# Kernel tuning notes

Hardware: AMD Instinct MI355X
Metric: run time of the kernel (lower is better)

## Reference

```python
import jax, jax.numpy as jnp
import numpy as np

B, N, D = 2, 2048, 1024
H, DH = 16, 64
DI = 4096
EPS = 1e-5
NEG_SLOPE = 0.01  # F.leaky_relu default


def _ln(x, g, b):
    mu = jnp.mean(x, axis=-1, keepdims=True)
    var = jnp.mean((x - mu) ** 2, axis=-1, keepdims=True)
    return (x - mu) * jax.lax.rsqrt(var + EPS) * g + b


def setup_inputs() -> dict:
    key = jax.random.key(0)
    ks = jax.random.split(key, 10)
    s = 0.02
    return {
        "Z": jax.random.normal(ks[0], (B, N, D), jnp.float32),
        "new_mask": jax.random.normal(ks[1], (B, N, N), jnp.float32),
        "mask": jax.random.uniform(ks[2], (B, N, N), jnp.float32),
        "ln1_g": jnp.ones((D,), jnp.float32),
        "ln1_b": jnp.zeros((D,), jnp.float32),
        "qkv_w": jax.random.normal(ks[3], (3 * D, D), jnp.float32) * s,
        "qkv_b": jnp.zeros((3 * D,), jnp.float32),
        "o_w": jax.random.normal(ks[4], (D, H * DH), jnp.float32) * s,
        "ln2_g": jnp.ones((D,), jnp.float32),
        "ln2_b": jnp.zeros((D,), jnp.float32),
        "p1_w": jax.random.normal(ks[5], (DI, D), jnp.float32) * s,
        "p1_b": jnp.zeros((DI,), jnp.float32),
        "p2_w": jax.random.normal(ks[6], (D, DI), jnp.float32) * s,
        "p2_b": jnp.zeros((D,), jnp.float32),
    }


def reference(Z, new_mask, mask, ln1_g, ln1_b, qkv_w, qkv_b, o_w, ln2_g, ln2_b, p1_w, p1_b, p2_w, p2_b):
    inp = Z
    Zn = _ln(Z, ln1_g, ln1_b)
    qkv = (Zn @ qkv_w.T + qkv_b).reshape(B, N, H, 3 * DH)
    # torch chunk order in the source: V, Q, K
    V, Q, K = jnp.split(qkv, 3, axis=3)  # each [B,N,H,DH]
    # scores: einsum('bnij,bmij->binm') == [B,H,N,N]
    W = jnp.einsum("bnhd,bmhd->bhnm", Q, K) / np.sqrt(DH) + new_mask[:, None]
    A = jax.nn.softmax(W, axis=3) * mask[:, None]
    attn = jnp.einsum("bhnm,bmhd->bnhd", A, V).reshape(B, N, D)
    attn = jnp.where(attn >= 0, attn, NEG_SLOPE * attn) @ o_w.T  # leaky_relu then o_net (no bias)
    Z1 = attn + inp
    Zn2 = _ln(Z1, ln2_g, ln2_b)
    h = jax.nn.relu(Zn2 @ p1_w.T + p1_b)
    return h @ p2_w.T + p2_b + Z1
```

## Files before the change

### kernel.cpp

```cpp
#include <hip/hip_runtime.h>

typedef unsigned short u16;
typedef __attribute__((ext_vector_type(8))) short bf16x8;
typedef __attribute__((ext_vector_type(4))) float f32x4;
typedef __attribute__((ext_vector_type(16))) float f32x16;
typedef __attribute__((ext_vector_type(4))) unsigned u32x4;

#define DEV static __device__ __forceinline__

DEV u16 f2bf(float f) {
    unsigned u = __float_as_uint(f);
    u += 0x7FFFu + ((u >> 16) & 1u);
    return (u16)(u >> 16);
}

typedef const __attribute__((address_space(1))) void* gas1_t;
typedef __attribute__((address_space(3))) void* gas3_t;

DEV void gl_lds16(const u16* g, u16* l) {
    __builtin_amdgcn_global_load_lds((gas1_t)g, (gas3_t)l, 16, 0, 0);
}

DEV unsigned cvtpk_bf16(float a, float b) {
    unsigned r;
    asm("v_cvt_pk_bf16_f32 %0, %1, %2" : "=v"(r) : "v"(a), "v"(b));
    return r;
}

DEV int sw8(int row, int chunk) { return row * 64 + ((chunk ^ (row & 7)) << 3); }

__global__ __launch_bounds__(256) void prep_all(const float* __restrict__ qkv_w,
                                                const float* __restrict__ o_w,
                                                const float* __restrict__ p1_w,
                                                const float* __restrict__ p2_w,
                                                const float* __restrict__ qkv_b,
                                                const float* __restrict__ nm,
                                                const float* __restrict__ pm,
                                                u16* __restrict__ qkvW,
                                                u16* __restrict__ oW,
                                                u16* __restrict__ p1W,
                                                u16* __restrict__ p2W,
                                                float* __restrict__ pbias,
                                                unsigned* __restrict__ Mp) {
    const int bid = blockIdx.x, t = threadIdx.x;
    if (bid < 3072) {
        int i = bid * 256 + t;
        int orow = i >> 8, cc = i & 255;
        int region = orow >> 10, rem = orow & 1023, h = rem >> 6, tt = rem & 63;
        int srow = h * 192 + region * 64 + tt;
        float4 v = ((const float4*)qkv_w)[srow * 256 + cc];
        ushort4 o;
        o.x = f2bf(v.x); o.y = f2bf(v.y); o.z = f2bf(v.z); o.w = f2bf(v.w);
        ((ushort4*)qkvW)[i] = o;
    } else if (bid < 4096) {
        int i = (bid - 3072) * 256 + t;
        float4 v = ((const float4*)o_w)[i];
        ushort4 o;
        o.x = f2bf(v.x); o.y = f2bf(v.y); o.z = f2bf(v.z); o.w = f2bf(v.w);
        ((ushort4*)oW)[i] = o;
    } else if (bid < 8192) {
        int i = (bid - 4096) * 256 + t;
        float4 v = ((const float4*)p1_w)[i];
        ushort4 o;
        o.x = f2bf(v.x); o.y = f2bf(v.y); o.z = f2bf(v.z); o.w = f2bf(v.w);
        ((ushort4*)p1W)[i] = o;
    } else if (bid < 12288) {
        int i = (bid - 8192) * 256 + t;
        float4 v = ((const float4*)p2_w)[i];
        ushort4 o;
        o.x = f2bf(v.x); o.y = f2bf(v.y); o.z = f2bf(v.z); o.w = f2bf(v.w);
        ((ushort4*)p2W)[i] = o;
    } else if (bid < 20480) {
        int i = (bid - 12288) * 256 + t;
        float4 a = ((const float4*)nm)[i];
        float4 b = ((const float4*)pm)[i];
        uint4 o;
        o.x = ((unsigned)f2bf(b.x) << 16) | f2bf(a.x * 1.4426950f);
        o.y = ((unsigned)f2bf(b.y) << 16) | f2bf(a.y * 1.4426950f);
        o.z = ((unsigned)f2bf(b.z) << 16) | f2bf(a.z * 1.4426950f);
        o.w = ((unsigned)f2bf(b.w) << 16) | f2bf(a.w * 1.4426950f);
        int e = i * 4;
        int bb = e >> 22;
        int rem = e & 4194303;
        int n = rem >> 11;
        int m = rem & 2047;
        int mt = m >> 5;
        int m5 = m & 31;
        int c = m5 >> 3;
        int hi = (m5 >> 2) & 1;
        size_t oi = (((size_t)(bb * 64 + mt) * 4 + c) * 2048 + n) * 2 + hi;
        ((uint4*)Mp)[oi] = o;
    } else {
#pragma unroll
        for (int k = 0; k < 12; k++) {
            int i = k * 256 + t;
            int region = i >> 10, rem = i & 1023, h = rem >> 6, tt = rem & 63;
            pbias[i] = qkv_b[h * 192 + region * 64 + tt];
        }
    }
}

__global__ __launch_bounds__(256) void ln_bf16(const float* __restrict__ x,
                                               const float* __restrict__ gam,
                                               const float* __restrict__ bet,
                                               u16* __restrict__ y) {
    const int row = blockIdx.x;
    const int t = threadIdx.x;
    const float4 v = ((const float4*)(x + (size_t)row * 1024))[t];
    float s = v.x + v.y + v.z + v.w;
    float ss = v.x * v.x + v.y * v.y + v.z * v.z + v.w * v.w;
#pragma unroll
    for (int o = 1; o < 64; o <<= 1) {
        s += __shfl_xor(s, o);
        ss += __shfl_xor(ss, o);
    }
    __shared__ float rs[4], rss[4];
    const int wave = t >> 6, lane = t & 63;
    if (lane == 0) { rs[wave] = s; rss[wave] = ss; }
    __syncthreads();
    const float tot = rs[0] + rs[1] + rs[2] + rs[3];
    const float totss = rss[0] + rss[1] + rss[2] + rss[3];
    const float mu = tot * (1.0f / 1024.0f);
    const float var = totss * (1.0f / 1024.0f) - mu * mu;
    const float rstd = rsqrtf(var + 1e-5f);
    const float4 g4 = ((const float4*)gam)[t];
    const float4 b4 = ((const float4*)bet)[t];
    ushort4 o;
    o.x = f2bf((v.x - mu) * rstd * g4.x + b4.x);
    o.y = f2bf((v.y - mu) * rstd * g4.y + b4.y);
    o.z = f2bf((v.z - mu) * rstd * g4.z + b4.z);
    o.w = f2bf((v.w - mu) * rstd * g4.w + b4.w);
    ((ushort4*)(y + (size_t)row * 1024))[t] = o;
}

__global__ __launch_bounds__(256) void ln2_comb4(const float* __restrict__ p0,
                                                 const float* __restrict__ p1,
                                                 const float* __restrict__ p2,
                                                 const float* __restrict__ p3,
                                                 const float* __restrict__ Z,
                                                 const float* __restrict__ gam,
                                                 const float* __restrict__ bet,
                                                 float* __restrict__ Z1,
                                                 u16* __restrict__ y) {
    const int row = blockIdx.x;
    const int t = threadIdx.x;
    const size_t off = (size_t)row * 256 + t;
    const float4 a = ((const float4*)p0)[off];
    const float4 c = ((const float4*)p1)[off];
    const float4 d = ((const float4*)p2)[off];
    const float4 e = ((const float4*)p3)[off];
    const float4 z = ((const float4*)Z)[off];
    float4 v;
    v.x = a.x + c.x + d.x + e.x + z.x;
    v.y = a.y + c.y + d.y + e.y + z.y;
    v.z = a.z + c.z + d.z + e.z + z.z;
    v.w = a.w + c.w + d.w + e.w + z.w;
    ((float4*)Z1)[off] = v;
    float s = v.x + v.y + v.z + v.w;
    float ss = v.x * v.x + v.y * v.y + v.z * v.z + v.w * v.w;
#pragma unroll
    for (int o = 1; o < 64; o <<= 1) {
        s += __shfl_xor(s, o);
        ss += __shfl_xor(ss, o);
    }
    __shared__ float rs[4], rss[4];
    const int wave = t >> 6, lane = t & 63;
    if (lane == 0) { rs[wave] = s; rss[wave] = ss; }
    __syncthreads();
    const float tot = rs[0] + rs[1] + rs[2] + rs[3];
    const float totss = rss[0] + rss[1] + rss[2] + rss[3];
    const float mu = tot * (1.0f / 1024.0f);
    const float var = totss * (1.0f / 1024.0f) - mu * mu;
    const float rstd = rsqrtf(var + 1e-5f);
    const float4 g4 = ((const float4*)gam)[t];
    const float4 b4 = ((const float4*)bet)[t];
    ushort4 o;
    o.x = f2bf((v.x - mu) * rstd * g4.x + b4.x);
    o.y = f2bf((v.y - mu) * rstd * g4.y + b4.y);
    o.z = f2bf((v.z - mu) * rstd * g4.z + b4.z);
    o.w = f2bf((v.w - mu) * rstd * g4.w + b4.w);
    ((ushort4*)(y + (size_t)row * 1024))[t] = o;
}

__global__ __launch_bounds__(256) void out_comb(const float* __restrict__ p0,
                                                const float* __restrict__ p1,
                                                const float* __restrict__ bias,
                                                const float* __restrict__ Z1,
                                                float* __restrict__ out) {
    int i = blockIdx.x * 256 + threadIdx.x;
    float4 a = ((const float4*)p0)[i];
    float4 c = ((const float4*)p1)[i];
    float4 z = ((const float4*)Z1)[i];
    float4 b = ((const float4*)bias)[i & 255];
    float4 o;
    o.x = a.x + c.x + z.x + b.x; o.y = a.y + c.y + z.y + b.y;
    o.z = a.z + c.z + z.z + b.z; o.w = a.w + c.w + z.w + b.w;
    ((float4*)out)[i] = o;
}

template <int EPI>
__global__ __launch_bounds__(256, 3) void gemm_bt(const u16* __restrict__ A,
                                                  const u16* __restrict__ Bt,
                                                  const float* __restrict__ bias,
                                                  void* __restrict__ out0,
                                                  void* __restrict__ out1,
                                                  void* __restrict__ out2,
                                                  int M, int N, int K, int ldk) {
    __shared__ __align__(16) u16 As[128 * 32];
    __shared__ __align__(16) u16 Bs[128 * 32];
    const int tid = threadIdx.x;
    const int wave = tid >> 6, lane = tid & 63;
    const int lhi = lane >> 4, llo = lane & 15;
    const int bx = blockIdx.x, by = blockIdx.y;
    const int kz = blockIdx.z * K;

    const int arow = wave * 32 + (lane >> 2);
    const int acol = (lane & 3) * 8;
    const u16* gA = A + (size_t)(by * 128 + arow) * ldk + kz + acol;
    const u16* gB = Bt + (size_t)(bx * 128 + arow) * ldk + kz + acol;
    u16* lA = As + wave * 1024 + lane * 8;
    u16* lB = Bs + wave * 1024 + lane * 8;

    const int wr = wave >> 1, wc = wave & 1;
    const f32x4 zero = {0.f, 0.f, 0.f, 0.f};
    f32x4 acc[4][4];
#pragma unroll
    for (int i = 0; i < 4; i++)
#pragma unroll
        for (int j = 0; j < 4; j++) acc[i][j] = zero;

    for (int k0 = 0; k0 < K; k0 += 32) {
        __syncthreads();
        gl_lds16(gA, lA);
        gl_lds16(gA + 16 * (size_t)ldk, lA + 512);
        gl_lds16(gB, lB);
        gl_lds16(gB + 16 * (size_t)ldk, lB + 512);
        gA += 32; gB += 32;
        __syncthreads();
        bf16x8 af[4], bfr[4];
#pragma unroll
        for (int i = 0; i < 4; i++)
            af[i] = *(const bf16x8*)(As + (wr * 64 + i * 16 + llo) * 32 + lhi * 8);
#pragma unroll
        for (int j = 0; j < 4; j++)
            bfr[j] = *(const bf16x8*)(Bs + (wc * 64 + j * 16 + llo) * 32 + lhi * 8);
#pragma unroll
        for (int i = 0; i < 4; i++)
#pragma unroll
            for (int j = 0; j < 4; j++)
                acc[i][j] = __builtin_amdgcn_mfma_f32_16x16x32_bf16(af[i], bfr[j], acc[i][j], 0, 0, 0);
    }

    const int rbase = by * 128 + wr * 64 + lhi * 4;
    const int cbase = bx * 128 + wc * 64 + llo;
    float* pout = nullptr;
    if constexpr (EPI == 4) {
        pout = (blockIdx.z < 2) ? ((float*)out0 + (size_t)blockIdx.z * M * N)
                                : ((float*)out1 + (size_t)(blockIdx.z - 2) * M * N);
    }
#pragma unroll
    for (int i = 0; i < 4; i++) {
#pragma unroll
        for (int j = 0; j < 4; j++) {
#pragma unroll
            for (int r = 0; r < 4; r++) {
                const int row = rbase + i * 16 + r;
                const int col = cbase + j * 16;
                float v = acc[i][j][r];
                if constexpr (EPI == 0) {
                    v += bias[col];
                    const int region = col >> 10;
                    const int c = col & 1023;
                    const int b = row >> 11, n = row & 2047;
                    if (region == 0) {
                        ((float*)out0)[(size_t)row * 1024 + c] = v;
                    } else {
                        const int h = c >> 6, t = c & 63;
                        u16* dst = (region == 1) ? (u16*)out1 : (u16*)out2;
                        dst[(((size_t)(b * 16 + h)) * 2048 + n) * 64 + t] = f2bf(v);
                    }
                } else if constexpr (EPI == 2) {
                    v += bias[col];
                    v = v > 0.f ? v : 0.f;
                    ((u16*)out0)[(size_t)row * N + col] = f2bf(v);
                } else {
                    pout[(size_t)row * N + col] = v;
                }
            }
        }
    }
}

__global__ __launch_bounds__(256) void vtrans(const float* __restrict__ Vsc,
                                              u16* __restrict__ Vt) {
    __shared__ u16 Ts[64 * 72];
    const int nt = blockIdx.x;
    const int bh = blockIdx.y;
    const int b = bh >> 4, h = bh & 15;
    const int t = threadIdx.x;
    const int n0 = nt * 64;
    const int nr = t >> 2;
    const int dq = (t & 3) * 16;
    const float* src = Vsc + ((size_t)(b * 2048 + n0 + nr)) * 1024 + h * 64 + dq;
    float4 v0 = ((const float4*)src)[0];
    float4 v1 = ((const float4*)src)[1];
    float4 v2 = ((const float4*)src)[2];
    float4 v3 = ((const float4*)src)[3];
    u16* c0 = Ts + nr;
    c0[(dq + 0) * 72]  = f2bf(v0.x); c0[(dq + 1) * 72]  = f2bf(v0.y);
    c0[(dq + 2) * 72]  = f2bf(v0.z); c0[(dq + 3) * 72]  = f2bf(v0.w);
    c0[(dq + 4) * 72]  = f2bf(v1.x); c0[(dq + 5) * 72]  = f2bf(v1.y);
    c0[(dq + 6) * 72]  = f2bf(v1.z); c0[(dq + 7) * 72]  = f2bf(v1.w);
    c0[(dq + 8) * 72]  = f2bf(v2.x); c0[(dq + 9) * 72]  = f2bf(v2.y);
    c0[(dq + 10) * 72] = f2bf(v2.z); c0[(dq + 11) * 72] = f2bf(v2.w);
    c0[(dq + 12) * 72] = f2bf(v3.x); c0[(dq + 13) * 72] = f2bf(v3.y);
    c0[(dq + 14) * 72] = f2bf(v3.z); c0[(dq + 15) * 72] = f2bf(v3.w);
    __syncthreads();
    const int d = t >> 2, n8 = (t & 3) * 16;
    u16* dstrow = Vt + ((size_t)bh * 64 + d) * 2048 + n0;
#pragma unroll
    for (int w = 0; w < 4; w++) {
        const int gi = (n8 >> 2) + w;
        const int g5 = gi & 7, blk = gi >> 3;
        const int pg = (g5 & 4) | ((g5 & 1) << 1) | ((g5 >> 1) & 1);
        *(uint2*)(dstrow + blk * 32 + pg * 4) = *(const uint2*)(Ts + d * 72 + n8 + w * 4);
    }
}

DEV void stage_kv(const u16* __restrict__ Kg, const u16* __restrict__ Vtg,
                  u16* ks, u16* vs, int bh, int m0, int wave, int lane) {
    const int l3 = lane >> 3, l7 = lane & 7;
    const int swcol = (l7 ^ l3) << 3;
#pragma unroll
    for (int s = 0; s < 2; s++) {
        const int row = wave * 16 + s * 8 + l3;
        gl_lds16(Kg + ((size_t)bh * 2048 + m0 + row) * 64 + swcol,
                 ks + wave * 1024 + s * 512 + lane * 8);
        gl_lds16(Vtg + ((size_t)bh * 64 + row) * 2048 + m0 + swcol,
                 vs + wave * 1024 + s * 512 + lane * 8);
    }
}

__global__ __launch_bounds__(256, 4) void attn_fused6(const u16* __restrict__ Qg,
                                                      const u16* __restrict__ Kg,
                                                      const u16* __restrict__ Vtg,
                                                      const unsigned* __restrict__ Mp,
                                                      u16* __restrict__ attnL) {
    __shared__ __align__(16) u16 Ks[2][64 * 64];
    __shared__ __align__(16) u16 Vs[2][64 * 64];
    __shared__ float lsh[2][32], lsh2[2][32];
    const int tid = threadIdx.x, wave = tid >> 6, lane = tid & 63;
    const int qh = wave & 1, wm = wave >> 1;
    const int hi = lane >> 5, l31 = lane & 31;
    const int pid = blockIdx.x;
    const int seq = pid >> 3;
    const int hh = seq & 15;
    const int g = (pid & 7) + (seq >> 4) * 8;
    const int b = g >> 5, qt = g & 31;
    const int bh = b * 16 + hh;
    const int q0 = qt * 64;

    stage_kv(Kg, Vtg, Ks[0], Vs[0], bh, 0, wave, lane);
    const int qrow = q0 + qh * 32 + l31;
    const u16* qptr = Qg + ((size_t)bh * 2048 + qrow) * 64 + hi * 8;
    bf16x8 qf[4];
#pragma unroll
    for (int ks = 0; ks < 4; ks++) qf[ks] = *(const bf16x8*)(qptr + ks * 16);

    const uint4* mb4 = (const uint4*)Mp + ((size_t)(b * 64 + wm) * 4) * 4096
                                        + (size_t)qrow * 2 + hi;

    const f32x16 z16 = {0.f,0.f,0.f,0.f,0.f,0.f,0.f,0.f,0.f,0.f,0.f,0.f,0.f,0.f,0.f,0.f};
    f32x16 accO[2];
    accO[0] = z16; accO[1] = z16;
    float lsum = 0.f;
    const float CS = 0.125f * 1.4426950f;
    __syncthreads();

    for (int t = 0; t < 32; t++) {
        const int cur = t & 1;
        const uint4* mp4 = mb4 + (size_t)t * 32768;
        const uint4 mva = mp4[0], mvb = mp4[4096], mvc = mp4[8192], mvd = mp4[12288];
        if (t < 31) stage_kv(Kg, Vtg, Ks[cur ^ 1], Vs[cur ^ 1], bh, (t + 1) * 64, wave, lane);

        const u16* ksb = Ks[cur];
        f32x16 sacc = z16;
        __builtin_amdgcn_s_setprio(1);
#pragma unroll
        for (int ks = 0; ks < 4; ks++) {
            const bf16x8 kf = *(const bf16x8*)(ksb + sw8(wm * 32 + l31, ks * 2 + hi));
            sacc = __builtin_amdgcn_mfma_f32_32x32x16_bf16(kf, qf[ks], sacc, 0, 0, 0);
        }
        __builtin_amdgcn_s_setprio(0);

        const unsigned mm[16] = {mva.x, mva.y, mva.z, mva.w, mvb.x, mvb.y, mvb.z, mvb.w,
                                 mvc.x, mvc.y, mvc.z, mvc.w, mvd.x, mvd.y, mvd.z, mvd.w};
        float p[16];
#pragma unroll
        for (int r = 0; r < 16; r++) {
            const unsigned u = mm[r];
            const float e = exp2f(fmaf(sacc[r], CS, __uint_as_float(u << 16)));
            lsum += e;
            p[r] = e * __uint_as_float(u & 0xFFFF0000u);
        }
        const u32x4 fa0 = {cvtpk_bf16(p[0], p[1]),  cvtpk_bf16(p[2], p[3]),
                           cvtpk_bf16(p[4], p[5]),  cvtpk_bf16(p[6], p[7])};
        const u32x4 fa1 = {cvtpk_bf16(p[8], p[9]),  cvtpk_bf16(p[10], p[11]),
                           cvtpk_bf16(p[12], p[13]), cvtpk_bf16(p[14], p[15])};
        const bf16x8 pa0 = __builtin_bit_cast(bf16x8, fa0);
        const bf16x8 pa1 = __builtin_bit_cast(bf16x8, fa1);

        const u16* vsb = Vs[cur];
        __builtin_amdgcn_s_setprio(1);
#pragma unroll
        for (int dh = 0; dh < 2; dh++) {
            const bf16x8 vf0 = *(const bf16x8*)(vsb + sw8(dh * 32 + l31, wm * 4 + hi));
            accO[dh] = __builtin_amdgcn_mfma_f32_32x32x16_bf16(pa0, vf0, accO[dh], 0, 0, 0);
            const bf16x8 vf1 = *(const bf16x8*)(vsb + sw8(dh * 32 + l31, wm * 4 + 2 + hi));
            accO[dh] = __builtin_amdgcn_mfma_f32_32x32x16_bf16(pa1, vf1, accO[dh], 0, 0, 0);
        }
        __builtin_amdgcn_s_setprio(0);
        __syncthreads();
    }

    const float lsum2 = lsum + __shfl_xor(lsum, 32);
    float* cb = (float*)&Ks[0][0];
    if (wm == 1) {
        float* dst = cb + (size_t)(qh * 64 + lane) * 32;
#pragma unroll
        for (int dh = 0; dh < 2; dh++)
#pragma unroll
            for (int c = 0; c < 4; c++) {
                const f32x4 v = {accO[dh][c * 4 + 0], accO[dh][c * 4 + 1],
                                 accO[dh][c * 4 + 2], accO[dh][c * 4 + 3]};
                *(f32x4*)(dst + dh * 16 + c * 4) = v;
            }
        if (lane < 32) lsh[qh][lane] = lsum2;
    }
    __syncthreads();
    if (wm == 0) {
        const float* src = cb + (size_t)(qh * 64 + lane) * 32;
        const float lt = lsum2 + lsh[qh][l31];
#pragma unroll
        for (int dh = 0; dh < 2; dh++)
#pragma unroll
            for (int c = 0; c < 16; c++)
                accO[dh][c] += src[dh * 16 + c];
        if (lane < 32) lsh2[qh][lane] = 1.0f / lt;
    }
    __syncthreads();
    if (wm == 0) {
#pragma unroll
        for (int r = 0; r < 16; r++) {
            const int ql = (r & 3) + 8 * (r >> 2) + 4 * hi;
            const float linv = lsh2[qh][ql];
            const int qg = q0 + qh * 32 + ql;
#pragma unroll
            for (int dh = 0; dh < 2; dh++) {
                float v = accO[dh][r] * linv;
                v = v >= 0.f ? v : 0.01f * v;
                attnL[((size_t)b * 2048 + qg) * 1024 + hh * 64 + dh * 32 + l31] = f2bf(v);
            }
        }
    }
}

extern "C" void kernel_launch(void* const* d_in, const int* in_sizes, int n_in,
                              void* d_out, int out_size, void* d_ws, size_t ws_size,
                              hipStream_t stream) {
    const float* Z     = (const float*)d_in[0];
    const float* nmask = (const float*)d_in[1];
    const float* pmask = (const float*)d_in[2];
    const float* ln1_g = (const float*)d_in[3];
    const float* ln1_b = (const float*)d_in[4];
    const float* qkv_w = (const float*)d_in[5];
    const float* qkv_b = (const float*)d_in[6];
    const float* o_w   = (const float*)d_in[7];
    const float* ln2_g = (const float*)d_in[8];
    const float* ln2_b = (const float*)d_in[9];
    const float* p1_w  = (const float*)d_in[10];
    const float* p1_b  = (const float*)d_in[11];
    const float* p2_w  = (const float*)d_in[12];
    const float* p2_b  = (const float*)d_in[13];
    float* out = (float*)d_out;

    char* w = (char*)d_ws;
    auto take = [&](size_t bytes) -> char* {
        char* p = w;
        w += (bytes + 255) & ~(size_t)255;
        return p;
    };
    u16* qkvW   = (u16*)take((size_t)3072 * 1024 * 2);
    u16* oW     = (u16*)take((size_t)1024 * 1024 * 2);
    u16* p1W    = (u16*)take((size_t)4096 * 1024 * 2);
    u16* p2W    = (u16*)take((size_t)1024 * 4096 * 2);
    u16* Zn     = (u16*)take((size_t)4096 * 1024 * 2);
    u16* Qb     = (u16*)take((size_t)32 * 2048 * 64 * 2);
    u16* Kb     = (u16*)take((size_t)32 * 2048 * 64 * 2);
    u16* Vt     = (u16*)take((size_t)32 * 64 * 2048 * 2);
    u16* attnL  = (u16*)take((size_t)4096 * 1024 * 2);
    float* Z1   = (float*)take((size_t)4096 * 1024 * 4);
    u16* hbuf   = (u16*)take((size_t)4096 * 4096 * 2);
    unsigned* Mp = (unsigned*)take((size_t)2 * 2048 * 2048 * 4);
    float* pbias = (float*)take((size_t)3072 * 4);
    float* Vsc    = (float*)hbuf;
    float* part01 = (float*)Mp;
    float* part23 = (float*)hbuf;

    prep_all<<<dim3(20481), 256, 0, stream>>>(qkv_w, o_w, p1_w, p2_w, qkv_b, nmask, pmask,
                                              qkvW, oW, p1W, p2W, pbias, Mp);
    ln_bf16<<<dim3(4096), 256, 0, stream>>>(Z, ln1_g, ln1_b, Zn);
    gemm_bt<0><<<dim3(24, 32), 256, 0, stream>>>(Zn, qkvW, pbias, Vsc, Qb, Kb, 4096, 3072, 1024, 1024);
    vtrans<<<dim3(32, 32), 256, 0, stream>>>(Vsc, Vt);
    attn_fused6<<<dim3(1024), 256, 0, stream>>>(Qb, Kb, Vt, Mp, attnL);
    gemm_bt<4><<<dim3(8, 32, 4), 256, 0, stream>>>(attnL, oW, nullptr, part01, part23, nullptr,
                                                   4096, 1024, 256, 1024);
    ln2_comb4<<<dim3(4096), 256, 0, stream>>>(part01, part01 + (size_t)4096 * 1024,
                                              part23, part23 + (size_t)4096 * 1024,
                                              Z, ln2_g, ln2_b, Z1, Zn);
    gemm_bt<2><<<dim3(32, 32), 256, 0, stream>>>(Zn, p1W, p1_b, hbuf, nullptr, nullptr,
                                                 4096, 4096, 1024, 1024);
    gemm_bt<4><<<dim3(8, 32, 2), 256, 0, stream>>>(hbuf, p2W, nullptr, part01, nullptr, nullptr,
                                                   4096, 1024, 2048, 4096);
    out_comb<<<dim3(4096), 256, 0, stream>>>(part01, part01 + (size_t)4096 * 1024, p2_b, Z1, out);
}
```

Measured before the change: 447.8 us.

## Fuse V transpose into QKV GEMM epilogue and restructure attention loop

The QKV GEMM epilogue now writes V directly as transposed, permuted bf16 into Vt, which removes the fp32 Vsc intermediate and the separate vtrans kernel. The attention kernel is unrolled by two with explicit double-buffered staging and mask prefetch one tile ahead. The additive mask is preloaded as the MFMA accumulator initial value, so the per-element fma is folded away. The mask is now prescaled by 8 instead of log2e, and the cross-wave combine uses an XOR-swizzled LDS layout to avoid bank conflicts. The risks are extra register pressure from the prefetched mask and possible precision changes from the new mask scaling.

```diff
diff --git a/kernel.cpp b/kernel.cpp
--- a/kernel.cpp
+++ b/kernel.cpp
@@ -2,6 +2,7 @@
 
 typedef unsigned short u16;
 typedef __attribute__((ext_vector_type(8))) short bf16x8;
+typedef __attribute__((ext_vector_type(2))) float f32x2;
 typedef __attribute__((ext_vector_type(4))) float f32x4;
 typedef __attribute__((ext_vector_type(16))) float f32x16;
 typedef __attribute__((ext_vector_type(4))) unsigned u32x4;
@@ -13,6 +14,8 @@
     u += 0x7FFFu + ((u >> 16) & 1u);
     return (u16)(u >> 16);
 }
+
+DEV float uaf(unsigned u) { return __uint_as_float(u); }
 
 typedef const __attribute__((address_space(1))) void* gas1_t;
 typedef __attribute__((address_space(3))) void* gas3_t;
@@ -75,10 +78,10 @@
         float4 a = ((const float4*)nm)[i];
         float4 b = ((const float4*)pm)[i];
         uint4 o;
-        o.x = ((unsigned)f2bf(b.x) << 16) | f2bf(a.x * 1.4426950f);
-        o.y = ((unsigned)f2bf(b.y) << 16) | f2bf(a.y * 1.4426950f);
-        o.z = ((unsigned)f2bf(b.z) << 16) | f2bf(a.z * 1.4426950f);
-        o.w = ((unsigned)f2bf(b.w) << 16) | f2bf(a.w * 1.4426950f);
+        o.x = ((unsigned)f2bf(b.x) << 16) | f2bf(a.x * 8.0f);
+        o.y = ((unsigned)f2bf(b.y) << 16) | f2bf(a.y * 8.0f);
+        o.z = ((unsigned)f2bf(b.z) << 16) | f2bf(a.z * 8.0f);
+        o.w = ((unsigned)f2bf(b.w) << 16) | f2bf(a.w * 8.0f);
         int e = i * 4;
         int bb = e >> 22;
         int rem = e & 4194303;
@@ -253,95 +256,77 @@
 
     const int rbase = by * 128 + wr * 64 + lhi * 4;
     const int cbase = bx * 128 + wc * 64 + llo;
-    float* pout = nullptr;
-    if constexpr (EPI == 4) {
-        pout = (blockIdx.z < 2) ? ((float*)out0 + (size_t)blockIdx.z * M * N)
-                                : ((float*)out1 + (size_t)(blockIdx.z - 2) * M * N);
-    }
-#pragma unroll
-    for (int i = 0; i < 4; i++) {
-#pragma unroll
-        for (int j = 0; j < 4; j++) {
-#pragma unroll
-            for (int r = 0; r < 4; r++) {
-                const int row = rbase + i * 16 + r;
-                const int col = cbase + j * 16;
-                float v = acc[i][j][r];
-                if constexpr (EPI == 0) {
-                    v += bias[col];
-                    const int region = col >> 10;
-                    const int c = col & 1023;
-                    const int b = row >> 11, n = row & 2047;
-                    if (region == 0) {
-                        ((float*)out0)[(size_t)row * 1024 + c] = v;
-                    } else {
+    if constexpr (EPI == 0) {
+        if (cbase < 1024) {
+#pragma unroll
+            for (int i = 0; i < 4; i++) {
+                const int row0 = rbase + i * 16;
+                const int bb = row0 >> 11, nn = row0 & 2047;
+                const int g5 = (nn >> 2) & 7;
+                const int pg = (g5 & 4) | ((g5 & 1) << 1) | ((g5 >> 1) & 1);
+                const int nnp = (nn & ~31) | (pg << 2);
+#pragma unroll
+                for (int j = 0; j < 4; j++) {
+                    const int col = cbase + j * 16;
+                    const float bv = bias[col];
+                    const int h = col >> 6, d = col & 63;
+                    ushort4 o4;
+                    o4.x = f2bf(acc[i][j][0] + bv);
+                    o4.y = f2bf(acc[i][j][1] + bv);
+                    o4.z = f2bf(acc[i][j][2] + bv);
+                    o4.w = f2bf(acc[i][j][3] + bv);
+                    *(ushort4*)((u16*)out0 + ((size_t)(bb * 16 + h) * 64 + d) * 2048 + nnp) = o4;
+                }
+            }
+        } else {
+#pragma unroll
+            for (int i = 0; i < 4; i++) {
+#pragma unroll
+                for (int j = 0; j < 4; j++) {
+#pragma unroll
+                    for (int r = 0; r < 4; r++) {
+                        const int row = rbase + i * 16 + r;
+                        const int col = cbase + j * 16;
+                        float v = acc[i][j][r] + bias[col];
+                        const int region = col >> 10;
+                        const int c = col & 1023;
+                        const int b = row >> 11, n = row & 2047;
                         const int h = c >> 6, t = c & 63;
                         u16* dst = (region == 1) ? (u16*)out1 : (u16*)out2;
                         dst[(((size_t)(b * 16 + h)) * 2048 + n) * 64 + t] = f2bf(v);
                     }
-                } else if constexpr (EPI == 2) {
-                    v += bias[col];
-                    v = v > 0.f ? v : 0.f;
-                    ((u16*)out0)[(size_t)row * N + col] = f2bf(v);
-                } else {
-                    pout[(size_t)row * N + col] = v;
                 }
             }
         }
-    }
-}
-
-__global__ __launch_bounds__(256) void vtrans(const float* __restrict__ Vsc,
-                                              u16* __restrict__ Vt) {
-    __shared__ u16 Ts[64 * 72];
-    const int nt = blockIdx.x;
-    const int bh = blockIdx.y;
-    const int b = bh >> 4, h = bh & 15;
-    const int t = threadIdx.x;
-    const int n0 = nt * 64;
-    const int nr = t >> 2;
-    const int dq = (t & 3) * 16;
-    const float* src = Vsc + ((size_t)(b * 2048 + n0 + nr)) * 1024 + h * 64 + dq;
-    float4 v0 = ((const float4*)src)[0];
-    float4 v1 = ((const float4*)src)[1];
-    float4 v2 = ((const float4*)src)[2];
-    float4 v3 = ((const float4*)src)[3];
-    u16* c0 = Ts + nr;
-    c0[(dq + 0) * 72]  = f2bf(v0.x); c0[(dq + 1) * 72]  = f2bf(v0.y);
-    c0[(dq + 2) * 72]  = f2bf(v0.z); c0[(dq + 3) * 72]  = f2bf(v0.w);
-    c0[(dq + 4) * 72]  = f2bf(v1.x); c0[(dq + 5) * 72]  = f2bf(v1.y);
-    c0[(dq + 6) * 72]  = f2bf(v1.z); c0[(dq + 7) * 72]  = f2bf(v1.w);
-    c0[(dq + 8) * 72]  = f2bf(v2.x); c0[(dq + 9) * 72]  = f2bf(v2.y);
-    c0[(dq + 10) * 72] = f2bf(v2.z); c0[(dq + 11) * 72] = f2bf(v2.w);
-    c0[(dq + 12) * 72] = f2bf(v3.x); c0[(dq + 13) * 72] = f2bf(v3.y);
-    c0[(dq + 14) * 72] = f2bf(v3.z); c0[(dq + 15) * 72] = f2bf(v3.w);
-    __syncthreads();
-    const int d = t >> 2, n8 = (t & 3) * 16;
-    u16* dstrow = Vt + ((size_t)bh * 64 + d) * 2048 + n0;
-#pragma unroll
-    for (int w = 0; w < 4; w++) {
-        const int gi = (n8 >> 2) + w;
-        const int g5 = gi & 7, blk = gi >> 3;
-        const int pg = (g5 & 4) | ((g5 & 1) << 1) | ((g5 >> 1) & 1);
-        *(uint2*)(dstrow + blk * 32 + pg * 4) = *(const uint2*)(Ts + d * 72 + n8 + w * 4);
-    }
-}
-
-DEV void stage_kv(const u16* __restrict__ Kg, const u16* __restrict__ Vtg,
-                  u16* ks, u16* vs, int bh, int m0, int wave, int lane) {
-    const int l3 = lane >> 3, l7 = lane & 7;
-    const int swcol = (l7 ^ l3) << 3;
-#pragma unroll
-    for (int s = 0; s < 2; s++) {
-        const int row = wave * 16 + s * 8 + l3;
-        gl_lds16(Kg + ((size_t)bh * 2048 + m0 + row) * 64 + swcol,
-                 ks + wave * 1024 + s * 512 + lane * 8);
-        gl_lds16(Vtg + ((size_t)bh * 64 + row) * 2048 + m0 + swcol,
-                 vs + wave * 1024 + s * 512 + lane * 8);
-    }
-}
-
-__global__ __launch_bounds__(256, 4) void attn_fused6(const u16* __restrict__ Qg,
+    } else {
+        float* pout = nullptr;
+        if constexpr (EPI == 4) {
+            pout = (blockIdx.z < 2) ? ((float*)out0 + (size_t)blockIdx.z * M * N)
+                                    : ((float*)out1 + (size_t)(blockIdx.z - 2) * M * N);
+        }
+#pragma unroll
+        for (int i = 0; i < 4; i++) {
+#pragma unroll
+            for (int j = 0; j < 4; j++) {
+#pragma unroll
+                for (int r = 0; r < 4; r++) {
+                    const int row = rbase + i * 16 + r;
+                    const int col = cbase + j * 16;
+                    float v = acc[i][j][r];
+                    if constexpr (EPI == 2) {
+                        v += bias[col];
+                        v = v > 0.f ? v : 0.f;
+                        ((u16*)out0)[(size_t)row * N + col] = f2bf(v);
+                    } else {
+                        pout[(size_t)row * N + col] = v;
+                    }
+                }
+            }
+        }
+    }
+}
+
+__global__ __launch_bounds__(256, 4) void attn_fused7(const u16* __restrict__ Qg,
                                                       const u16* __restrict__ Kg,
                                                       const u16* __restrict__ Vtg,
                                                       const unsigned* __restrict__ Mp,
@@ -360,7 +345,22 @@
     const int bh = b * 16 + hh;
     const int q0 = qt * 64;
 
-    stage_kv(Kg, Vtg, Ks[0], Vs[0], bh, 0, wave, lane);
+    const int l3 = lane >> 3, l7 = lane & 7;
+    const int swcol = (l7 ^ l3) << 3;
+    const int srow = wave * 16 + l3;
+    const u16* kp = Kg + ((size_t)bh * 2048 + srow) * 64 + swcol;
+    const u16* vp = Vtg + ((size_t)bh * 64 + srow) * 2048 + swcol;
+    u16* lKa = Ks[0] + wave * 1024 + lane * 8;
+    u16* lKb = Ks[1] + wave * 1024 + lane * 8;
+    u16* lVa = Vs[0] + wave * 1024 + lane * 8;
+    u16* lVb = Vs[1] + wave * 1024 + lane * 8;
+
+#define STAGE(LK, LV) do { \
+        gl_lds16(kp, LK); gl_lds16(kp + 512, (LK) + 512); \
+        gl_lds16(vp, LV); gl_lds16(vp + 16384, (LV) + 512); \
+        kp += 4096; vp += 64; } while (0)
+
+    STAGE(lKa, lVa);
     const int qrow = q0 + qh * 32 + l31;
     const u16* qptr = Qg + ((size_t)bh * 2048 + qrow) * 64 + hi * 8;
     bf16x8 qf[4];
@@ -369,83 +369,108 @@
 
     const uint4* mb4 = (const uint4*)Mp + ((size_t)(b * 64 + wm) * 4) * 4096
                                         + (size_t)qrow * 2 + hi;
+    uint4 mA0 = mb4[0], mA1 = mb4[4096], mA2 = mb4[8192], mA3 = mb4[12288];
+    uint4 mB0, mB1, mB2, mB3;
+    const uint4* mn = mb4 + 32768;
 
     const f32x16 z16 = {0.f,0.f,0.f,0.f,0.f,0.f,0.f,0.f,0.f,0.f,0.f,0.f,0.f,0.f,0.f,0.f};
     f32x16 accO[2];
     accO[0] = z16; accO[1] = z16;
-    float lsum = 0.f;
+    f32x2 lsv = {0.f, 0.f};
     const float CS = 0.125f * 1.4426950f;
     __syncthreads();
 
-    for (int t = 0; t < 32; t++) {
-        const int cur = t & 1;
-        const uint4* mp4 = mb4 + (size_t)t * 32768;
-        const uint4 mva = mp4[0], mvb = mp4[4096], mvc = mp4[8192], mvd = mp4[12288];
-        if (t < 31) stage_kv(Kg, Vtg, Ks[cur ^ 1], Vs[cur ^ 1], bh, (t + 1) * 64, wave, lane);
-
-        const u16* ksb = Ks[cur];
-        f32x16 sacc = z16;
-        __builtin_amdgcn_s_setprio(1);
-#pragma unroll
-        for (int ks = 0; ks < 4; ks++) {
-            const bf16x8 kf = *(const bf16x8*)(ksb + sw8(wm * 32 + l31, ks * 2 + hi));
-            sacc = __builtin_amdgcn_mfma_f32_32x32x16_bf16(kf, qf[ks], sacc, 0, 0, 0);
+#define QUAD(M, q) { \
+        f32x2 s0 = {sacc[q] * CS, sacc[q + 1] * CS}; \
+        f32x2 s1 = {sacc[q + 2] * CS, sacc[q + 3] * CS}; \
+        f32x2 e0 = {__builtin_amdgcn_exp2f(s0.x), __builtin_amdgcn_exp2f(s0.y)}; \
+        f32x2 e1 = {__builtin_amdgcn_exp2f(s1.x), __builtin_amdgcn_exp2f(s1.y)}; \
+        lsv += e0; lsv += e1; \
+        f32x2 pm0 = {uaf(M.x & 0xFFFF0000u), uaf(M.y & 0xFFFF0000u)}; \
+        f32x2 pm1 = {uaf(M.z & 0xFFFF0000u), uaf(M.w & 0xFFFF0000u)}; \
+        e0 *= pm0; e1 *= pm1; \
+        wpk[(q) / 2] = cvtpk_bf16(e0.x, e0.y); \
+        wpk[(q) / 2 + 1] = cvtpk_bf16(e1.x, e1.y); }
+
+#define ITER(KSB, VSB, M0, M1, M2, M3) do { \
+        f32x16 sacc; \
+        sacc[0] = uaf(M0.x << 16); sacc[1] = uaf(M0.y << 16); \
+        sacc[2] = uaf(M0.z << 16); sacc[3] = uaf(M0.w << 16); \
+        sacc[4] = uaf(M1.x << 16); sacc[5] = uaf(M1.y << 16); \
+        sacc[6] = uaf(M1.z << 16); sacc[7] = uaf(M1.w << 16); \
+        sacc[8] = uaf(M2.x << 16); sacc[9] = uaf(M2.y << 16); \
+        sacc[10] = uaf(M2.z << 16); sacc[11] = uaf(M2.w << 16); \
+        sacc[12] = uaf(M3.x << 16); sacc[13] = uaf(M3.y << 16); \
+        sacc[14] = uaf(M3.z << 16); sacc[15] = uaf(M3.w << 16); \
+        __builtin_amdgcn_s_setprio(1); \
+        _Pragma("unroll") \
+        for (int ks = 0; ks < 4; ks++) { \
+            const bf16x8 kf = *(const bf16x8*)((KSB) + sw8(wm * 32 + l31, ks * 2 + hi)); \
+            sacc = __builtin_amdgcn_mfma_f32_32x32x16_bf16(kf, qf[ks], sacc, 0, 0, 0); \
+        } \
+        __builtin_amdgcn_s_setprio(0); \
+        unsigned wpk[8]; \
+        QUAD(M0, 0) QUAD(M1, 4) QUAD(M2, 8) QUAD(M3, 12) \
+        const u32x4 fa0v = {wpk[0], wpk[1], wpk[2], wpk[3]}; \
+        const u32x4 fa1v = {wpk[4], wpk[5], wpk[6], wpk[7]}; \
+        const bf16x8 pa0 = __builtin_bit_cast(bf16x8, fa0v); \
+        const bf16x8 pa1 = __builtin_bit_cast(bf16x8, fa1v); \
+        __builtin_amdgcn_s_setprio(1); \
+        _Pragma("unroll") \
+        for (int dh = 0; dh < 2; dh++) { \
+            const bf16x8 vf0 = *(const bf16x8*)((VSB) + sw8(dh * 32 + l31, wm * 4 + hi)); \
+            accO[dh] = __builtin_amdgcn_mfma_f32_32x32x16_bf16(pa0, vf0, accO[dh], 0, 0, 0); \
+            const bf16x8 vf1 = *(const bf16x8*)((VSB) + sw8(dh * 32 + l31, wm * 4 + 2 + hi)); \
+            accO[dh] = __builtin_amdgcn_mfma_f32_32x32x16_bf16(pa1, vf1, accO[dh], 0, 0, 0); \
+        } \
+        __builtin_amdgcn_s_setprio(0); \
+        __syncthreads(); } while (0)
+
+    for (int tt = 0; tt < 16; tt++) {
+        mB0 = mn[0]; mB1 = mn[4096]; mB2 = mn[8192]; mB3 = mn[12288]; mn += 32768;
+        STAGE(lKb, lVb);
+        ITER(Ks[0], Vs[0], mA0, mA1, mA2, mA3);
+        if (tt < 15) {
+            mA0 = mn[0]; mA1 = mn[4096]; mA2 = mn[8192]; mA3 = mn[12288]; mn += 32768;
+            STAGE(lKa, lVa);
         }
-        __builtin_amdgcn_s_setprio(0);
-
-        const unsigned mm[16] = {mva.x, mva.y, mva.z, mva.w, mvb.x, mvb.y, mvb.z, mvb.w,
-                                 mvc.x, mvc.y, mvc.z, mvc.w, mvd.x, mvd.y, mvd.z, mvd.w};
-        float p[16];
-#pragma unroll
-        for (int r = 0; r < 16; r++) {
-            const unsigned u = mm[r];
-            const float e = exp2f(fmaf(sacc[r], CS, __uint_as_float(u << 16)));
-            lsum += e;
-            p[r] = e * __uint_as_float(u & 0xFFFF0000u);
-        }
-        const u32x4 fa0 = {cvtpk_bf16(p[0], p[1]),  cvtpk_bf16(p[2], p[3]),
-                           cvtpk_bf16(p[4], p[5]),  cvtpk_bf16(p[6], p[7])};
-        const u32x4 fa1 = {cvtpk_bf16(p[8], p[9]),  cvtpk_bf16(p[10], p[11]),
-                           cvtpk_bf16(p[12], p[13]), cvtpk_bf16(p[14], p[15])};
-        const bf16x8 pa0 = __builtin_bit_cast(bf16x8, fa0);
-        const bf16x8 pa1 = __builtin_bit_cast(bf16x8, fa1);
-
-        const u16* vsb = Vs[cur];
-        __builtin_amdgcn_s_setprio(1);
-#pragma unroll
-        for (int dh = 0; dh < 2; dh++) {
-            const bf16x8 vf0 = *(const bf16x8*)(vsb + sw8(dh * 32 + l31, wm * 4 + hi));
-            accO[dh] = __builtin_amdgcn_mfma_f32_32x32x16_bf16(pa0, vf0, accO[dh], 0, 0, 0);
-            const bf16x8 vf1 = *(const bf16x8*)(vsb + sw8(dh * 32 + l31, wm * 4 + 2 + hi));
-            accO[dh] = __builtin_amdgcn_mfma_f32_32x32x16_bf16(pa1, vf1, accO[dh], 0, 0, 0);
-        }
-        __builtin_amdgcn_s_setprio(0);
-        __syncthreads();
-    }
-
+        ITER(Ks[1], Vs[1], mB0, mB1, mB2, mB3);
+    }
+#undef ITER
+#undef QUAD
+#undef STAGE
+
+    const float lsum = lsv.x + lsv.y;
     const float lsum2 = lsum + __shfl_xor(lsum, 32);
     float* cb = (float*)&Ks[0][0];
+    const int slot = qh * 64 + lane;
+    const int s7 = slot & 7;
     if (wm == 1) {
-        float* dst = cb + (size_t)(qh * 64 + lane) * 32;
+        float* dst = cb + (size_t)slot * 32;
 #pragma unroll
         for (int dh = 0; dh < 2; dh++)
 #pragma unroll
             for (int c = 0; c < 4; c++) {
                 const f32x4 v = {accO[dh][c * 4 + 0], accO[dh][c * 4 + 1],
                                  accO[dh][c * 4 + 2], accO[dh][c * 4 + 3]};
-                *(f32x4*)(dst + dh * 16 + c * 4) = v;
+                *(f32x4*)(dst + (((dh * 4 + c) ^ s7) << 2)) = v;
             }
         if (lane < 32) lsh[qh][lane] = lsum2;
     }
     __syncthreads();
     if (wm == 0) {
-        const float* src = cb + (size_t)(qh * 64 + lane) * 32;
+        const float* src = cb + (size_t)slot * 32;
         const float lt = lsum2 + lsh[qh][l31];
 #pragma unroll
         for (int dh = 0; dh < 2; dh++)
 #pragma unroll
-            for (int c = 0; c < 16; c++)
-                accO[dh][c] += src[dh * 16 + c];
+            for (int c = 0; c < 4; c++) {
+                const f32x4 v = *(const f32x4*)(src + (((dh * 4 + c) ^ s7) << 2));
+                accO[dh][c * 4 + 0] += v.x;
+                accO[dh][c * 4 + 1] += v.y;
+                accO[dh][c * 4 + 2] += v.z;
+                accO[dh][c * 4 + 3] += v.w;
+            }
         if (lane < 32) lsh2[qh][lane] = 1.0f / lt;
     }
     __syncthreads();
@@ -503,16 +528,14 @@
     u16* hbuf   = (u16*)take((size_t)4096 * 4096 * 2);
     unsigned* Mp = (unsigned*)take((size_t)2 * 2048 * 2048 * 4);
     float* pbias = (float*)take((size_t)3072 * 4);
-    float* Vsc    = (float*)hbuf;
     float* part01 = (float*)Mp;
     float* part23 = (float*)hbuf;
 
     prep_all<<<dim3(20481), 256, 0, stream>>>(qkv_w, o_w, p1_w, p2_w, qkv_b, nmask, pmask,
                                               qkvW, oW, p1W, p2W, pbias, Mp);
     ln_bf16<<<dim3(4096), 256, 0, stream>>>(Z, ln1_g, ln1_b, Zn);
-    gemm_bt<0><<<dim3(24, 32), 256, 0, stream>>>(Zn, qkvW, pbias, Vsc, Qb, Kb, 4096, 3072, 1024, 1024);
-    vtrans<<<dim3(32, 32), 256, 0, stream>>>(Vsc, Vt);
-    attn_fused6<<<dim3(1024), 256, 0, stream>>>(Qb, Kb, Vt, Mp, attnL);
+    gemm_bt<0><<<dim3(24, 32), 256, 0, stream>>>(Zn, qkvW, pbias, Vt, Qb, Kb, 4096, 3072, 1024, 1024);
+    attn_fused7<<<dim3(1024), 256, 0, stream>>>(Qb, Kb, Vt, Mp, attnL);
     gemm_bt<4><<<dim3(8, 32, 4), 256, 0, stream>>>(attnL, oW, nullptr, part01, part23, nullptr,
                                                    4096, 1024, 256, 1024);
     ln2_comb4<<<dim3(4096), 256, 0, stream>>>(part01, part01 + (size_t)4096 * 1024,
```

Measured after the change: 467.7 us. +4.5%, slower.
